# Kernel tuning notes

Measured on AMD Instinct MI355X. Metric: run time of the kernel, lower is better.

## Reference

```python
import jax, jax.numpy as jnp
import numpy as np

N_EMBD = 768
HEAD_SIZE = 64
BLOCK_SIZE = 64

def setup_inputs() -> dict:
    key = jax.random.key(0)
    kx, kk, kq, kv = jax.random.split(key, 4)
    B, T = 2048, BLOCK_SIZE
    scale = 1.0 / np.sqrt(N_EMBD)
    x = jax.random.normal(kx, (B, T, N_EMBD), dtype=jnp.float32)
    # torch Linear(no bias): y = x @ W.T with W [out,in]; store as [in,out]
    Wk = jax.random.normal(kk, (N_EMBD, HEAD_SIZE), dtype=jnp.float32) * scale
    Wq = jax.random.normal(kq, (N_EMBD, HEAD_SIZE), dtype=jnp.float32) * scale
    Wv = jax.random.normal(kv, (N_EMBD, HEAD_SIZE), dtype=jnp.float32) * scale
    return {"x": x, "Wk": Wk, "Wq": Wq, "Wv": Wv}

def reference(x, Wk, Wq, Wv):
    B, T, C = x.shape
    k = jnp.einsum('btc,ch->bth', x, Wk)  # [B,T,H]
    q = jnp.einsum('btc,ch->bth', x, Wq)
    v = jnp.einsum('btc,ch->bth', x, Wv)
    scale = k.shape[-1] ** -0.5
    wei = jnp.einsum('bth,bsh->bts', q, k) * scale  # [B,T,T]
    causal = jnp.tril(jnp.ones((T, T), dtype=bool))
    wei = jnp.where(causal, wei, -jnp.inf)
    wei = jax.nn.softmax(wei, axis=-1)  # dropout p=0.0 is identity
    out = jnp.einsum('bts,bsh->bth', wei, v)  # [B,T,H]
    return out
```

## Files before the change

kernel.cpp:

```cpp
#include <hip/hip_runtime.h>


#define BATCHES 2048
#define SEQ 64
#define CDIM 768
#define HDIM 64
#define NCHUNK 24

typedef __bf16 bf16x8 __attribute__((ext_vector_type(8)));
typedef float f32x4v __attribute__((ext_vector_type(4)));
typedef unsigned short u16x8 __attribute__((ext_vector_type(8)));

__device__ __forceinline__ unsigned short f2bf(float f) {
  return __builtin_bit_cast(unsigned short, (__bf16)f);
}

__device__ __forceinline__ int swz(int row, int col) {
  return row * 64 + (col ^ ((row & 7) << 3));
}

__device__ __forceinline__ f32x4v mfma16(bf16x8 a, bf16x8 b, f32x4v c) {
  return __builtin_amdgcn_mfma_f32_16x16x32_bf16(a, b, c, 0, 0, 0);
}

__device__ __forceinline__ bf16x8 lds_frag(const unsigned short* p, int row, int col) {
  return __builtin_bit_cast(bf16x8, *reinterpret_cast<const u16x8*>(p + swz(row, col)));
}

__device__ __forceinline__ void gl_lds16(const void* g, void* l) {
  __builtin_amdgcn_global_load_lds(
      (const __attribute__((address_space(1))) void*)g,
      (__attribute__((address_space(3))) void*)l, 16, 0, 0);
}

__global__ __launch_bounds__(256) void prep_wt_kernel(
    const float* __restrict__ Wk, const float* __restrict__ Wq,
    const float* __restrict__ Wv, unsigned short* __restrict__ wt) {
  int i = blockIdx.x * 256 + threadIdx.x;
  if (i >= NCHUNK * 8192) return;
  int c = i >> 13;
  int r2 = i & 8191;
  int slot = r2 >> 3;
  if (slot >= 768) return;
  int e = r2 & 7;
  int row = slot >> 2;
  int p = slot & 3;
  int g = p ^ ((row >> 1) & 3);
  int k = c * 32 + g * 8 + e;
  int mat = row >> 6;
  int h = row & 63;
  const float* W = (mat == 0) ? Wq : ((mat == 1) ? Wk : Wv);
  wt[i] = f2bf(W[k * HDIM + h]);
}

__global__ __launch_bounds__(512) void head_fused_kernel(
    const float* __restrict__ x, const unsigned short* __restrict__ wt,
    float* __restrict__ out) {
  const int bid = blockIdx.x;
  const int tid = threadIdx.x;
  const int w = tid >> 6;
  const int ww = w & 3;
  const int bat = w >> 2;
  const int lane = tid & 63;
  const int lane15 = lane & 15;
  const int lhi = lane >> 4;

  __shared__ __align__(16) unsigned char smem[81920];

  const char* xsrc0;
  const char* xsrc1;
  {
    int s = w * 64 + lane;
    int row = s >> 3;
    int p = s & 7;
    size_t boff = row * (CDIM * 4) + ((p ^ (row & 7)) * 16);
    xsrc0 = (const char*)x + (size_t)(2 * bid + 0) * (SEQ * CDIM * 4) + boff;
    xsrc1 = (const char*)x + (size_t)(2 * bid + 1) * (SEQ * CDIM * 4) + boff;
  }
  const int xdst = (w * 64 + lane) * 16;

  const char* wsrc0 = (const char*)wt + ((0 * 512 + w * 64 + lane) * 16);
  const char* wsrc1 = (const char*)wt + ((1 * 512 + w * 64 + lane) * 16);
  const int wdst0 = (0 * 512 + w * 64 + lane) * 16;
  const int wdst1 = (1 * 512 + w * 64 + lane) * 16;

  #define STAGE_X(cn, B)                                                    \
    do {                                                                    \
      char* xbp = (char*)smem + (B) * 16384;                                \
      gl_lds16(xsrc0 + (cn) * 128, xbp + 0 * 8192 + xdst);                  \
      gl_lds16(xsrc1 + (cn) * 128, xbp + 1 * 8192 + xdst);                  \
    } while (0)
  #define STAGE_W(cn, B)                                                    \
    do {                                                                    \
      char* wbp = (char*)smem + 49152 + (B) * 16384;                        \
      gl_lds16(wsrc0 + (cn) * 16384, wbp + wdst0);                          \
      gl_lds16(wsrc1 + (cn) * 16384, wbp + wdst1);                          \
    } while (0)

  const f32x4v z4 = {0.f, 0.f, 0.f, 0.f};
  f32x4v accq[4], acck[4], accv[4];
  #pragma unroll
  for (int n = 0; n < 4; ++n) { accq[n] = z4; acck[n] = z4; accv[n] = z4; }

  const int arow = 16 * ww + lane15;
  const int ag0 = (lhi * 2) ^ (arow & 7);
  const int ag1 = (lhi * 2 + 1) ^ (arow & 7);
  const int batoff = bat * 8192;

  STAGE_W(0, 0);
  STAGE_X(0, 0);
  STAGE_W(1, 1);
  STAGE_X(1, 1);
  STAGE_X(2, 2);

  #pragma unroll
  for (int c = 0; c < NCHUNK; ++c) {
    if (c <= NCHUNK - 3)      asm volatile("s_waitcnt vmcnt(6)" ::: "memory");
    else if (c == NCHUNK - 2) asm volatile("s_waitcnt vmcnt(4)" ::: "memory");
    else                      asm volatile("s_waitcnt vmcnt(0)" ::: "memory");
    __builtin_amdgcn_s_barrier();

    {
      const float* xs = (const float*)((char*)smem + (c % 3) * 16384 + batoff);
      const unsigned short* ws =
          (const unsigned short*)((char*)smem + 49152 + (c & 1) * 16384);
      f32x4v xa = *reinterpret_cast<const f32x4v*>(xs + arow * 32 + ag0 * 4);
      f32x4v xb4 = *reinterpret_cast<const f32x4v*>(xs + arow * 32 + ag1 * 4);
      u16x8 ar;
      #pragma unroll
      for (int i = 0; i < 4; ++i) { ar[i] = f2bf(xa[i]); ar[4 + i] = f2bf(xb4[i]); }
      bf16x8 a = __builtin_bit_cast(bf16x8, ar);
      #pragma unroll
      for (int n = 0; n < 4; ++n) {
        int brq = 0 * HDIM + 16 * n + lane15;
        int bpq = lhi ^ ((brq >> 1) & 3);
        bf16x8 bq = __builtin_bit_cast(bf16x8,
            *reinterpret_cast<const u16x8*>(ws + brq * 32 + bpq * 8));
        accq[n] = mfma16(a, bq, accq[n]);
        int brk = 1 * HDIM + 16 * n + lane15;
        int bpk = lhi ^ ((brk >> 1) & 3);
        bf16x8 bk = __builtin_bit_cast(bf16x8,
            *reinterpret_cast<const u16x8*>(ws + brk * 32 + bpk * 8));
        acck[n] = mfma16(a, bk, acck[n]);
        int brv = 2 * HDIM + 16 * n + lane15;
        int bpv = lhi ^ ((brv >> 1) & 3);
        bf16x8 bv = __builtin_bit_cast(bf16x8,
            *reinterpret_cast<const u16x8*>(ws + brv * 32 + bpv * 8));
        accv[n] = mfma16(a, bv, accv[n]);
      }
    }

    asm volatile("s_waitcnt lgkmcnt(0)" ::: "memory");
    __builtin_amdgcn_s_barrier();

    if (c + 2 < NCHUNK) STAGE_W(c + 2, c & 1);
    if (c + 3 < NCHUNK) STAGE_X(c + 3, c % 3);
  }

  #undef STAGE_X
  #undef STAGE_W

  unsigned short* k_lds  = (unsigned short*)((char*)smem + bat * 24576);
  unsigned short* vT_lds = (unsigned short*)((char*)smem + bat * 24576 + 8192);
  unsigned short* qp_lds = (unsigned short*)((char*)smem + bat * 24576 + 16384);
  #pragma unroll
  for (int n = 0; n < 4; ++n) {
    int h = 16 * n + lane15;
    #pragma unroll
    for (int j = 0; j < 4; ++j) {
      int s = 16 * ww + lhi * 4 + j;
      k_lds[swz(s, h)] = f2bf(acck[n][j]);
      vT_lds[swz(h, s)] = f2bf(accv[n][j]);
      qp_lds[swz(s, h)] = f2bf(accq[n][j]);
    }
  }
  __syncthreads();

  const int trow = 16 * ww + lane15;
  bf16x8 aq0 = lds_frag(qp_lds, trow, lhi * 8);
  bf16x8 aq1 = lds_frag(qp_lds, trow, 32 + lhi * 8);
  f32x4v accS[4];
  #pragma unroll
  for (int n = 0; n < 4; ++n) accS[n] = z4;
  #pragma unroll
  for (int sB = 0; sB < 4; ++sB) {
    if (sB <= ww) {
      bf16x8 bk0 = lds_frag(k_lds, 16 * sB + lane15, lhi * 8);
      bf16x8 bk1 = lds_frag(k_lds, 16 * sB + lane15, 32 + lhi * 8);
      accS[sB] = mfma16(aq0, bk0, accS[sB]);
      accS[sB] = mfma16(aq1, bk1, accS[sB]);
    }
  }

  float rinv[4];
  #pragma unroll
  for (int j = 0; j < 4; ++j) {
    int t = 16 * ww + lhi * 4 + j;
    float zv[4];
    float m = -3.0e38f;
    #pragma unroll
    for (int sB = 0; sB < 4; ++sB) {
      int s = 16 * sB + lane15;
      float zz = (sB <= ww && s <= t) ? accS[sB][j] * 0.125f : -3.0e38f;
      zv[sB] = zz;
      m = fmaxf(m, zz);
    }
    #pragma unroll
    for (int off = 1; off < 16; off <<= 1) m = fmaxf(m, __shfl_xor(m, off));
    float sum = 0.f;
    float pv[4];
    #pragma unroll
    for (int sB = 0; sB < 4; ++sB) {
      float pe = __expf(zv[sB] - m);
      pv[sB] = pe;
      sum += pe;
    }
    #pragma unroll
    for (int off = 1; off < 16; off <<= 1) sum += __shfl_xor(sum, off);
    rinv[j] = 1.0f / sum;
    #pragma unroll
    for (int sB = 0; sB < 4; ++sB)
      qp_lds[swz(t, 16 * sB + lane15)] = f2bf(pv[sB]);
  }
  __syncthreads();

  f32x4v accO[4];
  #pragma unroll
  for (int n = 0; n < 4; ++n) accO[n] = z4;
  #pragma unroll
  for (int s0 = 0; s0 < 64; s0 += 32) {
    if (s0 <= 16 * ww + 15) {
      bf16x8 ap = lds_frag(qp_lds, trow, s0 + lhi * 8);
      #pragma unroll
      for (int n = 0; n < 4; ++n) {
        bf16x8 bv = lds_frag(vT_lds, 16 * n + lane15, s0 + lhi * 8);
        accO[n] = mfma16(ap, bv, accO[n]);
      }
    }
  }

  float* op = out + (size_t)(2 * bid + bat) * (SEQ * HDIM);
  #pragma unroll
  for (int n = 0; n < 4; ++n) {
    int h = 16 * n + lane15;
    #pragma unroll
    for (int j = 0; j < 4; ++j) {
      int t = 16 * ww + lhi * 4 + j;
      op[t * HDIM + h] = accO[n][j] * rinv[j];
    }
  }
}

extern "C" void kernel_launch(void* const* d_in, const int* in_sizes, int n_in,
                              void* d_out, int out_size, void* d_ws, size_t ws_size,
                              hipStream_t stream) {
  const float* x  = (const float*)d_in[0];
  const float* Wk = (const float*)d_in[1];
  const float* Wq = (const float*)d_in[2];
  const float* Wv = (const float*)d_in[3];
  float* out = (float*)d_out;
  unsigned short* wt = (unsigned short*)d_ws;

  hipLaunchKernelGGL(prep_wt_kernel, dim3((NCHUNK * 8192 + 255) / 256), dim3(256),
                     0, stream, Wk, Wq, Wv, wt);
  hipLaunchKernelGGL(head_fused_kernel, dim3(BATCHES / 2), dim3(512), 0, stream,
                     x, wt, out);
}
```

Before: 106.5 us.

## Process eight batches per block to reuse staged weight tiles across batches

Each block now handles eight sequences instead of two. Every wave converts four x fragments per chunk and reuses each loaded weight fragment across them, which cuts per-batch LDS weight reads and global weight traffic. The weight workspace is packed without padding, and the x/weight pipeline moves from triple to double buffering with much larger LDS tiles. The costs are a 48-accumulator register footprint, possible spilling, one block per CU, and a shallower prefetch depth for a bandwidth-bound stream.

```diff
diff --git a/kernel.cpp b/kernel.cpp
--- a/kernel.cpp
+++ b/kernel.cpp
@@ -6,6 +6,7 @@
 #define CDIM 768
 #define HDIM 64
 #define NCHUNK 24
+#define PB 8
 
 typedef __bf16 bf16x8 __attribute__((ext_vector_type(8)));
 typedef float f32x4v __attribute__((ext_vector_type(4)));
@@ -37,11 +38,10 @@
     const float* __restrict__ Wk, const float* __restrict__ Wq,
     const float* __restrict__ Wv, unsigned short* __restrict__ wt) {
   int i = blockIdx.x * 256 + threadIdx.x;
-  if (i >= NCHUNK * 8192) return;
-  int c = i >> 13;
-  int r2 = i & 8191;
+  if (i >= 3 * HDIM * CDIM) return;
+  int c = i / 6144;
+  int r2 = i - c * 6144;
   int slot = r2 >> 3;
-  if (slot >= 768) return;
   int e = r2 & 7;
   int row = slot >> 2;
   int p = slot & 3;
@@ -53,7 +53,7 @@
   wt[i] = f2bf(W[k * HDIM + h]);
 }
 
-__global__ __launch_bounds__(512) void head_fused_kernel(
+__global__ __launch_bounds__(512, 2) void head_fused_kernel(
     const float* __restrict__ x, const unsigned short* __restrict__ wt,
     float* __restrict__ out) {
   const int bid = blockIdx.x;
@@ -65,96 +65,110 @@
   const int lane15 = lane & 15;
   const int lhi = lane >> 4;
 
-  __shared__ __align__(16) unsigned char smem[81920];
-
-  const char* xsrc0;
-  const char* xsrc1;
-  {
-    int s = w * 64 + lane;
-    int row = s >> 3;
-    int p = s & 7;
-    size_t boff = row * (CDIM * 4) + ((p ^ (row & 7)) * 16);
-    xsrc0 = (const char*)x + (size_t)(2 * bid + 0) * (SEQ * CDIM * 4) + boff;
-    xsrc1 = (const char*)x + (size_t)(2 * bid + 1) * (SEQ * CDIM * 4) + boff;
-  }
-  const int xdst = (w * 64 + lane) * 16;
-
-  const char* wsrc0 = (const char*)wt + ((0 * 512 + w * 64 + lane) * 16);
-  const char* wsrc1 = (const char*)wt + ((1 * 512 + w * 64 + lane) * 16);
-  const int wdst0 = (0 * 512 + w * 64 + lane) * 16;
-  const int wdst1 = (1 * 512 + w * 64 + lane) * 16;
-
+  __shared__ __align__(16) unsigned char smem[155648];
+
+  const int xrow = tid >> 3;
+  const int xp = tid & 7;
+  const char* xbase = (const char*)x + (size_t)(PB * bid) * (SEQ * CDIM * 4) +
+                      xrow * (CDIM * 4) + ((xp ^ (xrow & 7)) * 16);
+  const int xdst = tid * 16;
+
+  const char* wbaseA = (const char*)wt + ((w * 64 + lane) * 16);
+  const char* wbaseB = (const char*)wt + (((8 + w) * 64 + lane) * 16);
+  const int wdstA = (w * 64 + lane) * 16;
+  const int wdstB = ((8 + w) * 64 + lane) * 16;
+
+  #define STAGE_W(cn, B)                                                    \
+    do {                                                                    \
+      char* wbp = (char*)smem + 131072 + (B) * 12288;                       \
+      gl_lds16(wbaseA + (cn) * 12288, wbp + wdstA);                         \
+      if (w < 4) gl_lds16(wbaseB + (cn) * 12288, wbp + wdstB);              \
+    } while (0)
   #define STAGE_X(cn, B)                                                    \
     do {                                                                    \
-      char* xbp = (char*)smem + (B) * 16384;                                \
-      gl_lds16(xsrc0 + (cn) * 128, xbp + 0 * 8192 + xdst);                  \
-      gl_lds16(xsrc1 + (cn) * 128, xbp + 1 * 8192 + xdst);                  \
+      char* xbp = (char*)smem + (B) * 65536;                                \
+      _Pragma("unroll")                                                     \
+      for (int i = 0; i < PB; ++i)                                          \
+        gl_lds16(xbase + (size_t)i * 196608 + (cn) * 128,                   \
+                 xbp + i * 8192 + xdst);                                    \
     } while (0)
-  #define STAGE_W(cn, B)                                                    \
-    do {                                                                    \
-      char* wbp = (char*)smem + 49152 + (B) * 16384;                        \
-      gl_lds16(wsrc0 + (cn) * 16384, wbp + wdst0);                          \
-      gl_lds16(wsrc1 + (cn) * 16384, wbp + wdst1);                          \
-    } while (0)
 
   const f32x4v z4 = {0.f, 0.f, 0.f, 0.f};
-  f32x4v accq[4], acck[4], accv[4];
+  f32x4v accq[4][4], acck[4][4], accv[4][4];
   #pragma unroll
-  for (int n = 0; n < 4; ++n) { accq[n] = z4; acck[n] = z4; accv[n] = z4; }
+  for (int s = 0; s < 4; ++s)
+    #pragma unroll
+    for (int n = 0; n < 4; ++n) { accq[s][n] = z4; acck[s][n] = z4; accv[s][n] = z4; }
 
   const int arow = 16 * ww + lane15;
   const int ag0 = (lhi * 2) ^ (arow & 7);
   const int ag1 = (lhi * 2 + 1) ^ (arow & 7);
-  const int batoff = bat * 8192;
 
   STAGE_W(0, 0);
   STAGE_X(0, 0);
   STAGE_W(1, 1);
   STAGE_X(1, 1);
-  STAGE_X(2, 2);
 
   #pragma unroll
   for (int c = 0; c < NCHUNK; ++c) {
-    if (c <= NCHUNK - 3)      asm volatile("s_waitcnt vmcnt(6)" ::: "memory");
-    else if (c == NCHUNK - 2) asm volatile("s_waitcnt vmcnt(4)" ::: "memory");
-    else                      asm volatile("s_waitcnt vmcnt(0)" ::: "memory");
+    if (c < NCHUNK - 1) {
+      if (w < 4) asm volatile("s_waitcnt vmcnt(10)" ::: "memory");
+      else       asm volatile("s_waitcnt vmcnt(9)" ::: "memory");
+    } else {
+      asm volatile("s_waitcnt vmcnt(0)" ::: "memory");
+    }
     __builtin_amdgcn_s_barrier();
 
-    {
-      const float* xs = (const float*)((char*)smem + (c % 3) * 16384 + batoff);
-      const unsigned short* ws =
-          (const unsigned short*)((char*)smem + 49152 + (c & 1) * 16384);
-      f32x4v xa = *reinterpret_cast<const f32x4v*>(xs + arow * 32 + ag0 * 4);
-      f32x4v xb4 = *reinterpret_cast<const f32x4v*>(xs + arow * 32 + ag1 * 4);
-      u16x8 ar;
-      #pragma unroll
-      for (int i = 0; i < 4; ++i) { ar[i] = f2bf(xa[i]); ar[4 + i] = f2bf(xb4[i]); }
-      bf16x8 a = __builtin_bit_cast(bf16x8, ar);
-      #pragma unroll
-      for (int n = 0; n < 4; ++n) {
-        int brq = 0 * HDIM + 16 * n + lane15;
-        int bpq = lhi ^ ((brq >> 1) & 3);
-        bf16x8 bq = __builtin_bit_cast(bf16x8,
-            *reinterpret_cast<const u16x8*>(ws + brq * 32 + bpq * 8));
-        accq[n] = mfma16(a, bq, accq[n]);
-        int brk = 1 * HDIM + 16 * n + lane15;
-        int bpk = lhi ^ ((brk >> 1) & 3);
-        bf16x8 bk = __builtin_bit_cast(bf16x8,
-            *reinterpret_cast<const u16x8*>(ws + brk * 32 + bpk * 8));
-        acck[n] = mfma16(a, bk, acck[n]);
-        int brv = 2 * HDIM + 16 * n + lane15;
-        int bpv = lhi ^ ((brv >> 1) & 3);
-        bf16x8 bv = __builtin_bit_cast(bf16x8,
-            *reinterpret_cast<const u16x8*>(ws + brv * 32 + bpv * 8));
-        accv[n] = mfma16(a, bv, accv[n]);
-      }
+    const char* xb = (const char*)smem + (c & 1) * 65536;
+    const unsigned short* wsb =
+        (const unsigned short*)((const char*)smem + 131072 + (c & 1) * 12288);
+
+    bf16x8 a0, a1, a2, a3;
+    #define LOAD_A(s, dst)                                                   \
+      do {                                                                   \
+        const float* xs = (const float*)(xb + (bat + 2 * (s)) * 8192);       \
+        f32x4v xa = *(const f32x4v*)(xs + arow * 32 + ag0 * 4);              \
+        f32x4v xb4 = *(const f32x4v*)(xs + arow * 32 + ag1 * 4);             \
+        u16x8 ar;                                                            \
+        _Pragma("unroll")                                                    \
+        for (int i = 0; i < 4; ++i) { ar[i] = f2bf(xa[i]); ar[4 + i] = f2bf(xb4[i]); } \
+        dst = __builtin_bit_cast(bf16x8, ar);                                \
+      } while (0)
+    LOAD_A(0, a0); LOAD_A(1, a1); LOAD_A(2, a2); LOAD_A(3, a3);
+    #undef LOAD_A
+
+    #pragma unroll
+    for (int n = 0; n < 4; ++n) {
+      int brq = 0 * HDIM + 16 * n + lane15;
+      int bpq = lhi ^ ((brq >> 1) & 3);
+      bf16x8 bq = __builtin_bit_cast(bf16x8,
+          *reinterpret_cast<const u16x8*>(wsb + brq * 32 + bpq * 8));
+      int brk = 1 * HDIM + 16 * n + lane15;
+      int bpk = lhi ^ ((brk >> 1) & 3);
+      bf16x8 bk = __builtin_bit_cast(bf16x8,
+          *reinterpret_cast<const u16x8*>(wsb + brk * 32 + bpk * 8));
+      int brv = 2 * HDIM + 16 * n + lane15;
+      int bpv = lhi ^ ((brv >> 1) & 3);
+      bf16x8 bv = __builtin_bit_cast(bf16x8,
+          *reinterpret_cast<const u16x8*>(wsb + brv * 32 + bpv * 8));
+      accq[0][n] = mfma16(a0, bq, accq[0][n]);
+      acck[0][n] = mfma16(a0, bk, acck[0][n]);
+      accv[0][n] = mfma16(a0, bv, accv[0][n]);
+      accq[1][n] = mfma16(a1, bq, accq[1][n]);
+      acck[1][n] = mfma16(a1, bk, acck[1][n]);
+      accv[1][n] = mfma16(a1, bv, accv[1][n]);
+      accq[2][n] = mfma16(a2, bq, accq[2][n]);
+      acck[2][n] = mfma16(a2, bk, acck[2][n]);
+      accv[2][n] = mfma16(a2, bv, accv[2][n]);
+      accq[3][n] = mfma16(a3, bq, accq[3][n]);
+      acck[3][n] = mfma16(a3, bk, acck[3][n]);
+      accv[3][n] = mfma16(a3, bv, accv[3][n]);
     }
 
     asm volatile("s_waitcnt lgkmcnt(0)" ::: "memory");
     __builtin_amdgcn_s_barrier();
 
-    if (c + 2 < NCHUNK) STAGE_W(c + 2, c & 1);
-    if (c + 3 < NCHUNK) STAGE_X(c + 3, c % 3);
+    if (c + 2 < NCHUNK) { STAGE_W(c + 2, c & 1); STAGE_X(c + 2, c & 1); }
   }
 
   #undef STAGE_X
@@ -163,91 +177,97 @@
   unsigned short* k_lds  = (unsigned short*)((char*)smem + bat * 24576);
   unsigned short* vT_lds = (unsigned short*)((char*)smem + bat * 24576 + 8192);
   unsigned short* qp_lds = (unsigned short*)((char*)smem + bat * 24576 + 16384);
+  const int trow = 16 * ww + lane15;
+  float* outbase = out + (size_t)(PB * bid + bat) * (SEQ * HDIM);
+
   #pragma unroll
-  for (int n = 0; n < 4; ++n) {
-    int h = 16 * n + lane15;
-    #pragma unroll
-    for (int j = 0; j < 4; ++j) {
-      int s = 16 * ww + lhi * 4 + j;
-      k_lds[swz(s, h)] = f2bf(acck[n][j]);
-      vT_lds[swz(h, s)] = f2bf(accv[n][j]);
-      qp_lds[swz(s, h)] = f2bf(accq[n][j]);
-    }
-  }
-  __syncthreads();
-
-  const int trow = 16 * ww + lane15;
-  bf16x8 aq0 = lds_frag(qp_lds, trow, lhi * 8);
-  bf16x8 aq1 = lds_frag(qp_lds, trow, 32 + lhi * 8);
-  f32x4v accS[4];
-  #pragma unroll
-  for (int n = 0; n < 4; ++n) accS[n] = z4;
-  #pragma unroll
-  for (int sB = 0; sB < 4; ++sB) {
-    if (sB <= ww) {
-      bf16x8 bk0 = lds_frag(k_lds, 16 * sB + lane15, lhi * 8);
-      bf16x8 bk1 = lds_frag(k_lds, 16 * sB + lane15, 32 + lhi * 8);
-      accS[sB] = mfma16(aq0, bk0, accS[sB]);
-      accS[sB] = mfma16(aq1, bk1, accS[sB]);
-    }
-  }
-
-  float rinv[4];
-  #pragma unroll
-  for (int j = 0; j < 4; ++j) {
-    int t = 16 * ww + lhi * 4 + j;
-    float zv[4];
-    float m = -3.0e38f;
+  for (int s = 0; s < 4; ++s) {
+    #pragma unroll
+    for (int n = 0; n < 4; ++n) {
+      int h = 16 * n + lane15;
+      #pragma unroll
+      for (int j = 0; j < 4; ++j) {
+        int srow = 16 * ww + lhi * 4 + j;
+        k_lds[swz(srow, h)] = f2bf(acck[s][n][j]);
+        vT_lds[swz(h, srow)] = f2bf(accv[s][n][j]);
+        qp_lds[swz(srow, h)] = f2bf(accq[s][n][j]);
+      }
+    }
+    __syncthreads();
+
+    bf16x8 aq0 = lds_frag(qp_lds, trow, lhi * 8);
+    bf16x8 aq1 = lds_frag(qp_lds, trow, 32 + lhi * 8);
+    f32x4v accS[4];
+    #pragma unroll
+    for (int n = 0; n < 4; ++n) accS[n] = z4;
     #pragma unroll
     for (int sB = 0; sB < 4; ++sB) {
-      int s = 16 * sB + lane15;
-      float zz = (sB <= ww && s <= t) ? accS[sB][j] * 0.125f : -3.0e38f;
-      zv[sB] = zz;
-      m = fmaxf(m, zz);
-    }
-    #pragma unroll
-    for (int off = 1; off < 16; off <<= 1) m = fmaxf(m, __shfl_xor(m, off));
-    float sum = 0.f;
-    float pv[4];
-    #pragma unroll
-    for (int sB = 0; sB < 4; ++sB) {
-      float pe = __expf(zv[sB] - m);
-      pv[sB] = pe;
-      sum += pe;
-    }
-    #pragma unroll
-    for (int off = 1; off < 16; off <<= 1) sum += __shfl_xor(sum, off);
-    rinv[j] = 1.0f / sum;
-    #pragma unroll
-    for (int sB = 0; sB < 4; ++sB)
-      qp_lds[swz(t, 16 * sB + lane15)] = f2bf(pv[sB]);
-  }
-  __syncthreads();
-
-  f32x4v accO[4];
-  #pragma unroll
-  for (int n = 0; n < 4; ++n) accO[n] = z4;
-  #pragma unroll
-  for (int s0 = 0; s0 < 64; s0 += 32) {
-    if (s0 <= 16 * ww + 15) {
-      bf16x8 ap = lds_frag(qp_lds, trow, s0 + lhi * 8);
-      #pragma unroll
-      for (int n = 0; n < 4; ++n) {
-        bf16x8 bv = lds_frag(vT_lds, 16 * n + lane15, s0 + lhi * 8);
-        accO[n] = mfma16(ap, bv, accO[n]);
-      }
-    }
-  }
-
-  float* op = out + (size_t)(2 * bid + bat) * (SEQ * HDIM);
-  #pragma unroll
-  for (int n = 0; n < 4; ++n) {
-    int h = 16 * n + lane15;
+      if (sB <= ww) {
+        bf16x8 bk0 = lds_frag(k_lds, 16 * sB + lane15, lhi * 8);
+        bf16x8 bk1 = lds_frag(k_lds, 16 * sB + lane15, 32 + lhi * 8);
+        accS[sB] = mfma16(aq0, bk0, accS[sB]);
+        accS[sB] = mfma16(aq1, bk1, accS[sB]);
+      }
+    }
+
+    float rinv[4];
     #pragma unroll
     for (int j = 0; j < 4; ++j) {
       int t = 16 * ww + lhi * 4 + j;
-      op[t * HDIM + h] = accO[n][j] * rinv[j];
-    }
+      float zv[4];
+      float m = -3.0e38f;
+      #pragma unroll
+      for (int sB = 0; sB < 4; ++sB) {
+        int sc = 16 * sB + lane15;
+        float zz = (sB <= ww && sc <= t) ? accS[sB][j] * 0.125f : -3.0e38f;
+        zv[sB] = zz;
+        m = fmaxf(m, zz);
+      }
+      #pragma unroll
+      for (int off = 1; off < 16; off <<= 1) m = fmaxf(m, __shfl_xor(m, off));
+      float sum = 0.f;
+      float pv[4];
+      #pragma unroll
+      for (int sB = 0; sB < 4; ++sB) {
+        float pe = __expf(zv[sB] - m);
+        pv[sB] = pe;
+        sum += pe;
+      }
+      #pragma unroll
+      for (int off = 1; off < 16; off <<= 1) sum += __shfl_xor(sum, off);
+      rinv[j] = 1.0f / sum;
+      #pragma unroll
+      for (int sB = 0; sB < 4; ++sB)
+        qp_lds[swz(t, 16 * sB + lane15)] = f2bf(pv[sB]);
+    }
+    __syncthreads();
+
+    f32x4v accO[4];
+    #pragma unroll
+    for (int n = 0; n < 4; ++n) accO[n] = z4;
+    #pragma unroll
+    for (int s0 = 0; s0 < 64; s0 += 32) {
+      if (s0 <= 16 * ww + 15) {
+        bf16x8 ap = lds_frag(qp_lds, trow, s0 + lhi * 8);
+        #pragma unroll
+        for (int n = 0; n < 4; ++n) {
+          bf16x8 bv = lds_frag(vT_lds, 16 * n + lane15, s0 + lhi * 8);
+          accO[n] = mfma16(ap, bv, accO[n]);
+        }
+      }
+    }
+
+    float* op = outbase + (size_t)(2 * s) * (SEQ * HDIM);
+    #pragma unroll
+    for (int n = 0; n < 4; ++n) {
+      int h = 16 * n + lane15;
+      #pragma unroll
+      for (int j = 0; j < 4; ++j) {
+        int t = 16 * ww + lhi * 4 + j;
+        op[t * HDIM + h] = accO[n][j] * rinv[j];
+      }
+    }
+    __syncthreads();
   }
 }
 
@@ -261,8 +281,8 @@
   float* out = (float*)d_out;
   unsigned short* wt = (unsigned short*)d_ws;
 
-  hipLaunchKernelGGL(prep_wt_kernel, dim3((NCHUNK * 8192 + 255) / 256), dim3(256),
+  hipLaunchKernelGGL(prep_wt_kernel, dim3((3 * HDIM * CDIM + 255) / 256), dim3(256),
                      0, stream, Wk, Wq, Wv, wt);
-  hipLaunchKernelGGL(head_fused_kernel, dim3(BATCHES / 2), dim3(512), 0, stream,
+  hipLaunchKernelGGL(head_fused_kernel, dim3(BATCHES / PB), dim3(512), 0, stream,
                      x, wt, out);
 }
```

After: 122.9 us. 15.4% more time.
